# Kernel optimization log

Measured on AMD Instinct MI355X. Metric: run time of the kernel, lower is better.

The kernel has to match this reference:

```python
import jax, jax.numpy as jnp
import numpy as np

L_LIST = [0, 1, 2, 3]
PAIRS = [(l1, l2) for l1 in L_LIST for l2 in L_LIST if l1 <= l2]
S, I, N = 8, 32, 8  # structures, atoms per structure, radial functions


def setup_inputs() -> dict:
    key = jax.random.key(0)
    inp = {}
    for l in L_LIST:
        key, k1, k2 = jax.random.split(key, 3)
        inp[f"c_in_l{l}"] = jax.random.normal(k1, (S, I, 2 * l + 1, N), dtype=jnp.float32)
        inp[f"c_tgt_l{l}"] = jax.random.normal(k2, (S, I, 2 * l + 1, N), dtype=jnp.float32)
    for (l1, l2) in PAIRS:
        key, k1 = jax.random.split(key)
        # overlap block stored pre-permuted: [S, i1, m1, n1, i2, m2, n2]
        inp[f"ovlp_l{l1}_l{l2}"] = jax.random.normal(
            k1, (S, I, 2 * l1 + 1, N, I, 2 * l2 + 1, N), dtype=jnp.float32)
    return inp


def _rho_loss(c_in, c_tgt, ovlp):
    # delta_coeffs = input - target, per (l) block (single species)
    d = {l: c_in[l] - c_tgt[l] for l in L_LIST}
    total = jnp.float32(0.0)
    for (l1, l2) in PAIRS:
        O = ovlp[(l1, l2)]
        # tensordot(c1, O, dims=3) over (i1, m1, n1), batched over structures s
        t = jnp.einsum('simn,simnjpq->sjpq', d[l1], O)
        # tensordot(t, c2, dims=3) over (i2, m2, n2), then sum over structures
        b = jnp.einsum('sjpq,sjpq->', t, d[l2])
        # diagonal blocks (l1==l2, a1==a2) counted once, off-diagonal twice
        total = total + (b if l1 == l2 else 2.0 * b)
    return total


def reference(c_in_l0, c_tgt_l0, c_in_l1, c_tgt_l1, c_in_l2, c_tgt_l2,
              c_in_l3, c_tgt_l3, ovlp_l0_l0, ovlp_l0_l1, ovlp_l0_l2,
              ovlp_l0_l3, ovlp_l1_l1, ovlp_l1_l2, ovlp_l1_l3, ovlp_l2_l2,
              ovlp_l2_l3, ovlp_l3_l3):
    c_in = {0: c_in_l0, 1: c_in_l1, 2: c_in_l2, 3: c_in_l3}
    c_tgt = {0: c_tgt_l0, 1: c_tgt_l1, 2: c_tgt_l2, 3: c_tgt_l3}
    ovlp = {(0, 0): ovlp_l0_l0, (0, 1): ovlp_l0_l1, (0, 2): ovlp_l0_l2,
            (0, 3): ovlp_l0_l3, (1, 1): ovlp_l1_l1, (1, 2): ovlp_l1_l2,
            (1, 3): ovlp_l1_l3, (2, 2): ovlp_l2_l2, (2, 3): ovlp_l2_l3,
            (3, 3): ovlp_l3_l3}
    return _rho_loss(c_in, c_tgt, ovlp)
```

## Files before the change

kernel.cpp:

```cpp
#include <hip/hip_runtime.h>


#define NUM_S 8

typedef float vfloat4 __attribute__((ext_vector_type(4)));

__device__ float g_d[32768];

__global__ __launch_bounds__(256) void compute_d_kernel(
    const float* __restrict__ ci0, const float* __restrict__ ct0,
    const float* __restrict__ ci1, const float* __restrict__ ct1,
    const float* __restrict__ ci2, const float* __restrict__ ct2,
    const float* __restrict__ ci3, const float* __restrict__ ct3,
    float* __restrict__ out) {
    const int t = blockIdx.x * 256 + threadIdx.x;
    if (t == 0) *out = 0.0f;
    float v;
    if (t < 2048)       v = ci0[t]         - ct0[t];
    else if (t < 8192)  v = ci1[t - 2048]  - ct1[t - 2048];
    else if (t < 18432) v = ci2[t - 8192]  - ct2[t - 8192];
    else                v = ci3[t - 18432] - ct3[t - 18432];
    g_d[t] = v;
}

template <int K1, int K2, int W, int NWP>
__device__ __forceinline__ float pair_rows(const float* __restrict__ O,
                                           const float* __restrict__ d1,
                                           const float* __restrict__ d2,
                                           int lw, int lane) {
    constexpr int C2q    = K2 / 4;
    constexpr int ROUNDS = C2q / 64;
    constexpr int NROWS  = NUM_S * K1;

    const int r_beg = (int)(((long long)lw * NROWS) / NWP);
    const int r_end = (int)(((long long)(lw + 1) * NROWS) / NWP);

    const vfloat4* __restrict__ O4 = (const vfloat4*)O;

    float ax = 0.f, ay = 0.f, az = 0.f, aw = 0.f;

    int t = r_beg;
    while (t < r_end) {
        const int s        = t / K1;
        const int seg_full = (s + 1) * K1;
        const int seg_end  = seg_full < r_end ? seg_full : r_end;

        const vfloat4* __restrict__ v = (const vfloat4*)(d2 + s * K2) + lane;
        vfloat4 vv[ROUNDS];
#pragma unroll
        for (int j = 0; j < ROUNDS; ++j) vv[j] = v[j * 64];

#pragma unroll 2
        for (int u = t; u < seg_end; ++u) {
            const vfloat4* __restrict__ o = O4 + (size_t)u * C2q + lane;
            vfloat4 ov[ROUNDS];
#pragma unroll
            for (int j = 0; j < ROUNDS; ++j)
                ov[j] = __builtin_nontemporal_load(o + j * 64);

            const float dd = d1[u];

            float dx = 0.f, dy = 0.f, dz = 0.f, dw = 0.f;
#pragma unroll
            for (int j = 0; j < ROUNDS; ++j) {
                dx = fmaf(ov[j].x, vv[j].x, dx);
                dy = fmaf(ov[j].y, vv[j].y, dy);
                dz = fmaf(ov[j].z, vv[j].z, dz);
                dw = fmaf(ov[j].w, vv[j].w, dw);
            }
            ax = fmaf(dd, dx, ax);
            ay = fmaf(dd, dy, ay);
            az = fmaf(dd, dz, az);
            aw = fmaf(dd, dw, aw);
        }
        t = seg_end;
    }
    return (float)W * ((ax + ay) + (az + aw));
}

__global__ __launch_bounds__(256) void rho_loss_kernel(
    const float* __restrict__ O00, const float* __restrict__ O01,
    const float* __restrict__ O02, const float* __restrict__ O03,
    const float* __restrict__ O11, const float* __restrict__ O12,
    const float* __restrict__ O13, const float* __restrict__ O22,
    const float* __restrict__ O23, const float* __restrict__ O33,
    float* __restrict__ out) {
    const int lane = threadIdx.x & 63;
    const int wid  = blockIdx.x * 4 + (threadIdx.x >> 6);

    const float* D0 = g_d;
    const float* D1 = g_d + 2048;
    const float* D2 = g_d + 8192;
    const float* D3 = g_d + 18432;

    float acc;
    if      (wid <   47) acc = pair_rows< 256,  256, 1,   47>(O00, D0, D0, wid,        lane);
    else if (wid <  192) acc = pair_rows< 256,  768, 2,  145>(O01, D0, D1, wid -   47, lane);
    else if (wid <  433) acc = pair_rows< 256, 1280, 2,  241>(O02, D0, D2, wid -  192, lane);
    else if (wid <  770) acc = pair_rows< 256, 1792, 2,  337>(O03, D0, D3, wid -  433, lane);
    else if (wid < 1204) acc = pair_rows< 768,  768, 1,  434>(O11, D1, D1, wid -  770, lane);
    else if (wid < 1927) acc = pair_rows< 768, 1280, 2,  723>(O12, D1, D2, wid - 1204, lane);
    else if (wid < 2939) acc = pair_rows< 768, 1792, 2, 1012>(O13, D1, D3, wid - 1927, lane);
    else if (wid < 4144) acc = pair_rows<1280, 1280, 1, 1205>(O22, D2, D2, wid - 2939, lane);
    else if (wid < 5831) acc = pair_rows<1280, 1792, 2, 1687>(O23, D2, D3, wid - 4144, lane);
    else                 acc = pair_rows<1792, 1792, 1, 2361>(O33, D3, D3, wid - 5831, lane);

    for (int off = 32; off > 0; off >>= 1)
        acc += __shfl_down(acc, off, 64);

    __shared__ float wsum[4];
    const int lwid = threadIdx.x >> 6;
    if (lane == 0) wsum[lwid] = acc;
    __syncthreads();
    if (threadIdx.x == 0) {
        float s = wsum[0] + wsum[1] + wsum[2] + wsum[3];
        atomicAdd(out, s);
    }
}

extern "C" void kernel_launch(void* const* d_in, const int* in_sizes, int n_in,
                              void* d_out, int out_size, void* d_ws, size_t ws_size,
                              hipStream_t stream) {
    (void)in_sizes; (void)n_in; (void)d_ws; (void)ws_size; (void)out_size;

    const float* ci0 = (const float*)d_in[0];
    const float* ct0 = (const float*)d_in[1];
    const float* ci1 = (const float*)d_in[2];
    const float* ct1 = (const float*)d_in[3];
    const float* ci2 = (const float*)d_in[4];
    const float* ct2 = (const float*)d_in[5];
    const float* ci3 = (const float*)d_in[6];
    const float* ct3 = (const float*)d_in[7];
    const float* O00 = (const float*)d_in[8];
    const float* O01 = (const float*)d_in[9];
    const float* O02 = (const float*)d_in[10];
    const float* O03 = (const float*)d_in[11];
    const float* O11 = (const float*)d_in[12];
    const float* O12 = (const float*)d_in[13];
    const float* O13 = (const float*)d_in[14];
    const float* O22 = (const float*)d_in[15];
    const float* O23 = (const float*)d_in[16];
    const float* O33 = (const float*)d_in[17];

    compute_d_kernel<<<128, 256, 0, stream>>>(ci0, ct0, ci1, ct1,
                                              ci2, ct2, ci3, ct3,
                                              (float*)d_out);

    rho_loss_kernel<<<2048, 256, 0, stream>>>(
        O00, O01, O02, O03, O11, O12, O13, O22, O23, O33, (float*)d_out);
}
```

Baseline: 318.3 us.

## Replace static wave partition with sharded atomic work-stealing queue

Splits the overlap rows into 12288 finer units spread over 8 sharded atomic counters. The 2048 blocks take initial units statically, then waves fetch further units dynamically until each shard's queue is empty. The aim is to even out load across waves and CUs for this bandwidth-bound reduction. In exchange it adds atomic traffic and per-unit segment setup, and the counters are reset by the preceding kernel.

New measurement: 324.4 us. No clear change (+1.9%).

```diff
diff --git a/kernel.cpp b/kernel.cpp
--- a/kernel.cpp
+++ b/kernel.cpp
@@ -6,6 +6,10 @@
 typedef float vfloat4 __attribute__((ext_vector_type(4)));
 
 __device__ float g_d[32768];
+__device__ __attribute__((aligned(128))) unsigned g_ctrs[8][32];
+
+#define NV_PER_SHARD 1536u
+#define Q_PER_SHARD  1024u
 
 __global__ __launch_bounds__(256) void compute_d_kernel(
     const float* __restrict__ ci0, const float* __restrict__ ct0,
@@ -15,6 +19,7 @@
     float* __restrict__ out) {
     const int t = blockIdx.x * 256 + threadIdx.x;
     if (t == 0) *out = 0.0f;
+    if (t < 8) g_ctrs[t][0] = Q_PER_SHARD;
     float v;
     if (t < 2048)       v = ci0[t]         - ct0[t];
     else if (t < 8192)  v = ci1[t - 2048]  - ct1[t - 2048];
@@ -78,6 +83,30 @@
     return (float)W * ((ax + ay) + (az + aw));
 }
 
+__device__ __forceinline__ float do_unit(
+    unsigned v, int lane,
+    const float* __restrict__ O00, const float* __restrict__ O01,
+    const float* __restrict__ O02, const float* __restrict__ O03,
+    const float* __restrict__ O11, const float* __restrict__ O12,
+    const float* __restrict__ O13, const float* __restrict__ O22,
+    const float* __restrict__ O23, const float* __restrict__ O33) {
+    const float* D0 = g_d;
+    const float* D1 = g_d + 2048;
+    const float* D2 = g_d + 8192;
+    const float* D3 = g_d + 18432;
+
+    if      (v <    72u) return pair_rows< 256,  256, 1,   72>(O00, D0, D0, (int)v,           lane);
+    else if (v <   289u) return pair_rows< 256,  768, 2,  217>(O01, D0, D1, (int)(v -   72), lane);
+    else if (v <   650u) return pair_rows< 256, 1280, 2,  361>(O02, D0, D2, (int)(v -  289), lane);
+    else if (v <  1156u) return pair_rows< 256, 1792, 2,  506>(O03, D0, D3, (int)(v -  650), lane);
+    else if (v <  1806u) return pair_rows< 768,  768, 1,  650>(O11, D1, D1, (int)(v - 1156), lane);
+    else if (v <  2890u) return pair_rows< 768, 1280, 2, 1084>(O12, D1, D2, (int)(v - 1806), lane);
+    else if (v <  4408u) return pair_rows< 768, 1792, 2, 1518>(O13, D1, D3, (int)(v - 2890), lane);
+    else if (v <  6215u) return pair_rows<1280, 1280, 1, 1807>(O22, D2, D2, (int)(v - 4408), lane);
+    else if (v <  8745u) return pair_rows<1280, 1792, 2, 2530>(O23, D2, D3, (int)(v - 6215), lane);
+    else                 return pair_rows<1792, 1792, 1, 3543>(O33, D3, D3, (int)(v - 8745), lane);
+}
+
 __global__ __launch_bounds__(256) void rho_loss_kernel(
     const float* __restrict__ O00, const float* __restrict__ O01,
     const float* __restrict__ O02, const float* __restrict__ O03,
@@ -85,31 +114,29 @@
     const float* __restrict__ O13, const float* __restrict__ O22,
     const float* __restrict__ O23, const float* __restrict__ O33,
     float* __restrict__ out) {
-    const int lane = threadIdx.x & 63;
-    const int wid  = blockIdx.x * 4 + (threadIdx.x >> 6);
+    const int lane  = threadIdx.x & 63;
+    const int lwid  = threadIdx.x >> 6;
+    const unsigned shard = blockIdx.x & 7u;
+    const unsigned q     = (blockIdx.x >> 3) * 4u + (unsigned)lwid;
 
-    const float* D0 = g_d;
-    const float* D1 = g_d + 2048;
-    const float* D2 = g_d + 8192;
-    const float* D3 = g_d + 18432;
+    float acc = 0.f;
+    unsigned u = 8u * q + shard;
+    for (;;) {
+        unsigned k = 0xffffffffu;
+        if (lane == 0) k = atomicAdd(&g_ctrs[shard][0], 1u);
 
-    float acc;
-    if      (wid <   47) acc = pair_rows< 256,  256, 1,   47>(O00, D0, D0, wid,        lane);
-    else if (wid <  192) acc = pair_rows< 256,  768, 2,  145>(O01, D0, D1, wid -   47, lane);
-    else if (wid <  433) acc = pair_rows< 256, 1280, 2,  241>(O02, D0, D2, wid -  192, lane);
-    else if (wid <  770) acc = pair_rows< 256, 1792, 2,  337>(O03, D0, D3, wid -  433, lane);
-    else if (wid < 1204) acc = pair_rows< 768,  768, 1,  434>(O11, D1, D1, wid -  770, lane);
-    else if (wid < 1927) acc = pair_rows< 768, 1280, 2,  723>(O12, D1, D2, wid - 1204, lane);
-    else if (wid < 2939) acc = pair_rows< 768, 1792, 2, 1012>(O13, D1, D3, wid - 1927, lane);
-    else if (wid < 4144) acc = pair_rows<1280, 1280, 1, 1205>(O22, D2, D2, wid - 2939, lane);
-    else if (wid < 5831) acc = pair_rows<1280, 1792, 2, 1687>(O23, D2, D3, wid - 4144, lane);
-    else                 acc = pair_rows<1792, 1792, 1, 2361>(O33, D3, D3, wid - 5831, lane);
+        acc += do_unit(u, lane, O00, O01, O02, O03, O11, O12, O13,
+                       O22, O23, O33);
+
+        k = (unsigned)__shfl((int)k, 0, 64);
+        if (k >= NV_PER_SHARD) break;
+        u = 8u * k + shard;
+    }
 
     for (int off = 32; off > 0; off >>= 1)
         acc += __shfl_down(acc, off, 64);
 
     __shared__ float wsum[4];
-    const int lwid = threadIdx.x >> 6;
     if (lane == 0) wsum[lwid] = acc;
     __syncthreads();
     if (threadIdx.x == 0) {
```
